# Performance work log

Measured on AMD Instinct MI355X. Metric: run time of the kernel, lower is better.

## Reference

```python
import jax, jax.numpy as jnp
import numpy as np

N, F, DEG, C = 20000, 64, 16, 16   # nodes, features, in-degree incl. self loop, classes
E = N * (DEG - 1)                   # regular (non-self-loop) edges


def setup_inputs() -> dict:
    key = jax.random.key(0)
    ks = jax.random.split(key, 12)
    x = jax.random.normal(ks[0], (N, F), dtype=jnp.float32)
    src = jax.random.randint(ks[1], (E,), 0, N, dtype=jnp.int32)
    dst = jnp.repeat(jnp.arange(N, dtype=jnp.int32), DEG - 1)  # exactly DEG-1 in-edges/node
    edge_index = jnp.stack([src, dst])
    s = 1.0 / np.sqrt(F)
    params = {}
    for i, kw, kb in ((1, ks[2], ks[3]), (2, ks[4], ks[5]), (3, ks[6], ks[7])):
        params[f"W{i}"] = jax.random.normal(kw, (F, F), dtype=jnp.float32) * s
        params[f"b{i}"] = jax.random.normal(kb, (F,), dtype=jnp.float32) * s
    params["Wfc"] = jax.random.normal(ks[8], (C, F), dtype=jnp.float32) * s
    params["bfc"] = jax.random.normal(ks[9], (C,), dtype=jnp.float32) * s
    return {"x": x, "edge_index": edge_index, **params}


def _pca_conv(h, src, dst, W, b):
    # GCNConv.forward: linear first, then propagate with symmetric normalization.
    hl = h @ W.T                                             # [N, F]
    # add self loops (appended after regular edges, as in PyG)
    loop = jnp.arange(N, dtype=src.dtype)
    src_a = jnp.concatenate([src, loop])
    dst_a = jnp.concatenate([dst, loop])
    deg = jnp.zeros((N,), hl.dtype).at[dst_a].add(1.0)
    dinv = jax.lax.rsqrt(deg)
    norm = dinv[src_a] * dinv[dst_a]                         # [Ea]
    m = norm[:, None] * hl[src_a]                            # messages [Ea, F]
    # aggregate(): pack each destination's messages contiguously, in edge order
    order = jnp.argsort(dst_a)                               # stable sort by destination
    sd = dst_a[order]
    slot = jnp.arange(sd.shape[0]) - jnp.searchsorted(sd, sd, side='left')
    neigh = jnp.zeros((N, DEG, F), hl.dtype).at[sd, slot].set(m[order])
    neigh = neigh.reshape(N, DEG * F)                        # [N, max_degree*F]
    # torch.pca_lowrank(neigh, q=F, center=True): top-F right singular vectors of
    # the column-centered matrix; computed via eigh on the (DEG*F x DEG*F) Gram.
    Xc = neigh - jnp.mean(neigh, axis=0, keepdims=True)
    G = Xc.T @ Xc                                            # [DEG*F, DEG*F]
    _, V = jnp.linalg.eigh(G)                                # ascending eigenvalues
    Vtop = V[:, ::-1][:, :F]                                 # top-F principal directions
    proj = neigh @ Vtop                                      # note: projects UNcentered neigh
    return proj @ W.T + b                                    # self.lin again + bias


def reference(x, edge_index, W1, b1, W2, b2, W3, b3, Wfc, bfc):
    src, dst = edge_index[0], edge_index[1]
    h = jax.nn.relu(_pca_conv(x, src, dst, W1, b1))
    h = jax.nn.relu(_pca_conv(h, src, dst, W2, b2))
    h = jax.nn.relu(_pca_conv(h, src, dst, W3, b3))
    out = h @ Wfc.T + bfc
    return jax.nn.log_softmax(out, axis=-1)
```

## Files before the change

kernel.cpp:

```cpp
#include <hip/hip_runtime.h>
#include <cmath>

#define NNODES 20000
#define FD 64
#define EPN 15
#define NB 1024
#define BSUB 80
#define NCLS 16
#define NPAIR 40

__global__ __launch_bounds__(256) void k_linT(const float* __restrict__ X,
    const float* __restrict__ W, const float* __restrict__ bias,
    float* __restrict__ out, int ncol, int relu)
{
  __shared__ float Wsh[64][65];
  __shared__ float Xsh[64][65];
  int t = threadIdx.x;
  int r0 = blockIdx.x * 64;
  for (int idx = t; idx < ncol * 64; idx += 256) Wsh[idx >> 6][idx & 63] = W[idx];
  for (int idx = t; idx < 64 * 64; idx += 256) {
    int r = idx >> 6, c = idx & 63;
    Xsh[r][c] = (r0 + r < NNODES) ? X[(size_t)(r0 + r) * 64 + c] : 0.f;
  }
  __syncthreads();
  for (int idx = t; idx < 64 * ncol; idx += 256) {
    int r = idx / ncol, o = idx % ncol;
    float acc = 0.f;
    #pragma unroll
    for (int j = 0; j < 64; j++) acc += Xsh[r][j] * Wsh[o][j];
    if (bias) acc += bias[o];
    if (relu) acc = fmaxf(acc, 0.f);
    if (r0 + r < NNODES) out[(size_t)(r0 + r) * ncol + o] = acc;
  }
}

__global__ __launch_bounds__(256) void k_meanslot(const float* __restrict__ hl,
    const int* __restrict__ src, float* __restrict__ mus)
{
  int k = blockIdx.x;
  int part = blockIdx.y;
  int t = threadIdx.x;
  int c = t & 63, sub = t >> 6;
  int d0 = part * 2500;
  float acc = 0.f;
  for (int d = d0 + sub; d < d0 + 2500; d += 4) {
    int row = (k < EPN) ? src[d * EPN + k] : d;
    acc += hl[(size_t)row * 64 + c];
  }
  __shared__ float red[4][64];
  red[sub][c] = acc;
  __syncthreads();
  if (t < 64) {
    float s = red[0][t] + red[1][t] + red[2][t] + red[3][t];
    atomicAdd(&mus[k * 64 + t], s * (1.f / 20000.f));
  }
}

__global__ __launch_bounds__(256) void k_buildX(const float* __restrict__ hl,
    const int* __restrict__ src, const float* __restrict__ mus,
    float* __restrict__ X)
{
  __shared__ float4 mu4[256];
  int t = threadIdx.x;
  int d0 = blockIdx.x * 64;
  mu4[t] = ((const float4*)mus)[t];
  __syncthreads();
  for (int k = 0; k < 16; k++) {
    for (int item = t; item < 1024; item += 256) {
      int rr = item >> 4, f4 = item & 15;
      int d = d0 + rr;
      if (d < NNODES) {
        int row = (k < EPN) ? src[d * EPN + k] : d;
        float4 v = ((const float4*)hl)[(size_t)row * 16 + f4];
        float4 m = mu4[k * 16 + f4];
        v.x -= m.x; v.y -= m.y; v.z -= m.z; v.w -= m.w;
        ((float4*)X)[(size_t)d * 256 + k * 16 + f4] = v;
      }
    }
  }
}

__global__ __launch_bounds__(256) void k_syrkX(const float* __restrict__ X,
    float* __restrict__ TP, int rows)
{
  __shared__ float As[32][128];
  __shared__ float Bs[32][128];
  int t = threadIdx.x;
  int pr = blockIdx.x, I = 0, rem = pr;
  for (int ii = 0; ii < 8; ii++) {
    int cnt = 8 - ii;
    if (rem < cnt) { I = ii; break; }
    rem -= cnt;
  }
  int J = I + rem;
  int d0 = blockIdx.y * rows;
  int d1 = d0 + rows;
  int a0 = (t & 15) * 4, b0 = (t >> 4) * 4;
  float4 pa[4], pb[4];
  auto LOADR = [&](int dc) {
    #pragma unroll
    for (int s = 0; s < 4; s++) {
      int idx = t + s * 256;
      int rr = idx >> 5, c4 = idx & 31;
      int d = dc + rr;
      float4 va = make_float4(0.f, 0.f, 0.f, 0.f), vb = va;
      if (d < d1) {
        va = ((const float4*)X)[(size_t)d * 256 + I * 32 + c4];
        vb = ((const float4*)X)[(size_t)d * 256 + J * 32 + c4];
      }
      pa[s] = va; pb[s] = vb;
    }
  };
  LOADR(d0);
  float acc[8][8] = {};
  for (int dc = d0; dc < d1; dc += 32) {
    __syncthreads();
    #pragma unroll
    for (int s = 0; s < 4; s++) {
      int idx = t + s * 256;
      int rr = idx >> 5, c4 = idx & 31;
      *(float4*)&As[rr][c4 * 4] = pa[s];
      *(float4*)&Bs[rr][c4 * 4] = pb[s];
    }
    __syncthreads();
    if (dc + 32 < d1) LOADR(dc + 32);
    for (int dd = 0; dd < 32; dd++) {
      float av[8], bv[8];
      *(float4*)&av[0] = *(const float4*)&As[dd][a0];
      *(float4*)&av[4] = *(const float4*)&As[dd][a0 + 64];
      *(float4*)&bv[0] = *(const float4*)&Bs[dd][b0];
      *(float4*)&bv[4] = *(const float4*)&Bs[dd][b0 + 64];
      #pragma unroll
      for (int x = 0; x < 8; x++)
        #pragma unroll
        for (int y = 0; y < 8; y++) acc[x][y] += av[x] * bv[y];
    }
  }
  float* Tout = TP + (size_t)blockIdx.y * ((size_t)NB * NB);
  #pragma unroll
  for (int x = 0; x < 8; x++) {
    int rowi = I * 128 + ((x < 4) ? (a0 + x) : (64 + a0 + x - 4));
    size_t base = (size_t)rowi * NB + J * 128;
    *(float4*)&Tout[base + b0]      = make_float4(acc[x][0], acc[x][1], acc[x][2], acc[x][3]);
    *(float4*)&Tout[base + 64 + b0] = make_float4(acc[x][4], acc[x][5], acc[x][6], acc[x][7]);
  }
}

__global__ __launch_bounds__(256) void k_assembleG16(const float* __restrict__ TP,
    float* __restrict__ G, int ns, float scale)
{
  size_t idx = (size_t)blockIdx.x * 256 + threadIdx.x;
  int p = (int)(idx >> 10), q = (int)(idx & 1023);
  int ti = p >> 6, tj = q >> 6;
  size_t e = (ti <= tj) ? idx : (((size_t)q << 10) | (size_t)p);
  float v = 0.f;
  for (int s2 = 0; s2 < ns; s2++) v += TP[(size_t)s2 * ((size_t)NB * NB) + e];
  G[idx] = v * scale;
}

__global__ __launch_bounds__(256) void k_gram(const float* __restrict__ hl,
    const int* __restrict__ src, const float* __restrict__ mus,
    float* __restrict__ T)
{
  __shared__ float Ash[64][64];
  __shared__ float Bsh[64][64];
  __shared__ float muA[64], muB[64];
  int t = threadIdx.x;
  int pr = blockIdx.x, i = 0, rem = pr;
  for (int ii = 0; ii < 16; ii++) {
    int cnt = 16 - ii;
    if (rem < cnt) { i = ii; break; }
    rem -= cnt;
  }
  int j = i + rem;
  if (t < 64) muA[t] = mus[i * 64 + t];
  else if (t < 128) muB[t - 64] = mus[j * 64 + (t - 64)];
  float acc[4][4] = {};
  int a0 = (t & 15) * 4, b0 = (t >> 4) * 4;
  int d0 = blockIdx.y * 4000, d1 = d0 + 4000;
  for (int dc = d0; dc < d1; dc += 64) {
    __syncthreads();
    for (int item = t; item < 1024; item += 256) {
      int rr = item >> 4, f4 = item & 15;
      int d = dc + rr;
      float4 va = make_float4(0.f, 0.f, 0.f, 0.f);
      float4 vb = va;
      if (d < d1) {
        int ra = (i < EPN) ? src[d * EPN + i] : d;
        int rb = (j < EPN) ? src[d * EPN + j] : d;
        va = ((const float4*)hl)[(size_t)ra * 16 + f4];
        vb = ((const float4*)hl)[(size_t)rb * 16 + f4];
        int cb = f4 * 4;
        va.x -= muA[cb]; va.y -= muA[cb + 1]; va.z -= muA[cb + 2]; va.w -= muA[cb + 3];
        vb.x -= muB[cb]; vb.y -= muB[cb + 1]; vb.z -= muB[cb + 2]; vb.w -= muB[cb + 3];
      }
      ((float4*)&Ash[rr][0])[f4] = va;
      ((float4*)&Bsh[rr][0])[f4] = vb;
    }
    __syncthreads();
    for (int dd = 0; dd < 64; dd++) {
      float av[4], bv[4];
      #pragma unroll
      for (int u = 0; u < 4; u++) av[u] = Ash[dd][a0 + u];
      #pragma unroll
      for (int u = 0; u < 4; u++) bv[u] = Bsh[dd][b0 + u];
      #pragma unroll
      for (int x = 0; x < 4; x++)
        #pragma unroll
        for (int y = 0; y < 4; y++) acc[x][y] += av[x] * bv[y];
    }
  }
  #pragma unroll
  for (int x = 0; x < 4; x++)
    #pragma unroll
    for (int y = 0; y < 4; y++)
      atomicAdd(&T[(size_t)(i * 64 + a0 + x) * NB + (j * 64 + b0 + y)], acc[x][y]);
}

__global__ __launch_bounds__(256) void k_assembleG(const float* __restrict__ T,
    float* __restrict__ G)
{
  size_t idx = (size_t)blockIdx.x * 256 + threadIdx.x;
  int p = (int)(idx >> 10), q = (int)(idx & 1023);
  int ti = p >> 6, tj = q >> 6;
  float v = (ti <= tj) ? T[idx] : T[((size_t)q << 10) | (size_t)p];
  G[idx] = v * (1.f / 256.f);
}

__global__ __launch_bounds__(256) void k_gemmG2(const float* __restrict__ G,
    float* __restrict__ G2)
{
  __shared__ float Ash[64][68];
  __shared__ float Bsh[64][68];
  int t = threadIdx.x;
  int bi = blockIdx.x * 64, bj = blockIdx.y * 64;
  int a0 = (t & 15) * 4, b0 = (t >> 4) * 4;
  float acc[4][4] = {};
  for (int d0 = 0; d0 < NB; d0 += 64) {
    __syncthreads();
    for (int item = t; item < 1024; item += 256) {
      int rr = item >> 4, f4 = item & 15;
      *(float4*)&Ash[rr][f4 * 4] =
          ((const float4*)G)[(size_t)(d0 + rr) * 256 + (bi >> 2) + f4];
      *(float4*)&Bsh[rr][f4 * 4] =
          ((const float4*)G)[(size_t)(d0 + rr) * 256 + (bj >> 2) + f4];
    }
    __syncthreads();
    for (int dd = 0; dd < 64; dd++) {
      float av[4], bv[4];
      #pragma unroll
      for (int u = 0; u < 4; u++) av[u] = Ash[dd][a0 + u];
      #pragma unroll
      for (int u = 0; u < 4; u++) bv[u] = Bsh[dd][b0 + u];
      #pragma unroll
      for (int x = 0; x < 4; x++)
        #pragma unroll
        for (int y = 0; y < 4; y++) acc[x][y] += av[x] * bv[y];
    }
  }
  #pragma unroll
  for (int x = 0; x < 4; x++) {
    float4 v = make_float4(acc[x][0], acc[x][1], acc[x][2], acc[x][3]);
    ((float4*)G2)[(size_t)(bi + a0 + x) * 256 + ((bj + b0) >> 2)] = v;
  }
}

__global__ void k_initScut(float* __restrict__ S, const float* __restrict__ G,
                           double* __restrict__ scal)
{
  int b = blockIdx.x;
  int t = threadIdx.x;
  if (b == 0) {
    __shared__ float red[256];
    float m = 0.f;
    for (int p = t; p < NB; p += 256) m = fmaxf(m, G[(size_t)p * NB + p]);
    red[t] = m;
    __syncthreads();
    for (int s = 128; s; s >>= 1) {
      if (t < s) red[t] = fmaxf(red[t], red[t + s]);
      __syncthreads();
    }
    if (t == 0) {
      double c = 0.9 * (double)red[0];
      scal[0] = c;
      scal[1] = c * c;
    }
    return;
  }
  int idx = (b - 1) * 256 + t;
  if (idx < NB * BSUB) {
    unsigned u = (unsigned)(idx + 1) * 2654435761u;
    u ^= u >> 16; u *= 2246822519u; u ^= u >> 13; u *= 3266489917u; u ^= u >> 16;
    S[idx] = ((float)u * (1.f / 4294967296.f)) - 0.5f;
  }
}

__global__ __launch_bounds__(256) void k_gzfused(const float* __restrict__ G,
    const float* __restrict__ Z, const float* __restrict__ Zp,
    float* __restrict__ P, float* __restrict__ out, int* __restrict__ cnt,
    const double* __restrict__ cptr, float s1, float s2, float s3)
{
  __shared__ float Gs[32][68];
  __shared__ float Zs[64][84];
  __shared__ int lastf;
  int t = threadIdx.x;
  int r0b = blockIdx.x;
  int r0 = r0b * 32;
  int kz = blockIdx.y;
  int cg_ = t & 15, rg = t >> 4;
  float acc0[5] = {}, acc1[5] = {};
  for (int k0 = kz * 128; k0 < kz * 128 + 128; k0 += 64) {
    __syncthreads();
    #pragma unroll
    for (int s = 0; s < 2; s++) {
      int item = t + s * 256;
      int rr = item >> 4, f4 = item & 15;
      float4 g = ((const float4*)G)[(size_t)(r0 + rr) * 256 + (k0 >> 2) + f4];
      *(float4*)&Gs[rr][f4 * 4] = g;
    }
    #pragma unroll
    for (int s = 0; s < 5; s++) {
      int item = t + s * 256;
      int rr = item / 20, f4 = item % 20;
      float4 z = ((const float4*)Z)[(size_t)(k0 + rr) * 20 + f4];
      *(float4*)&Zs[rr][f4 * 4] = z;
    }
    __syncthreads();
    for (int kk = 0; kk < 64; kk++) {
      float g0 = Gs[rg * 2 + 0][kk];
      float g1 = Gs[rg * 2 + 1][kk];
      float z[5];
      #pragma unroll
      for (int m = 0; m < 5; m++) z[m] = Zs[kk][cg_ * 5 + m];
      #pragma unroll
      for (int m = 0; m < 5; m++) { acc0[m] += g0 * z[m]; acc1[m] += g1 * z[m]; }
    }
  }
  size_t base = (size_t)kz * (NB * BSUB) + (size_t)(r0 + rg * 2) * BSUB + cg_ * 5;
  #pragma unroll
  for (int m = 0; m < 5; m++) P[base + m] = acc0[m];
  #pragma unroll
  for (int m = 0; m < 5; m++) P[base + BSUB + m] = acc1[m];
  __threadfence();
  __syncthreads();
  if (t == 0) {
    int old = atomicAdd(&cnt[r0b], 1);
    lastf = (old == 7) ? 1 : 0;
  }
  __syncthreads();
  if (!lastf) return;
  __threadfence();
  float coef = s1;
  if (cptr) coef = s1 * (float)(2.0 / cptr[0]);
  const float4* P4 = (const float4*)P;
  for (int idx = t; idx < 640; idx += 256) {
    size_t o4 = (size_t)r0 * 20 + idx;
    float4 a = P4[o4];
    #pragma unroll
    for (int u = 1; u < 8; u++) {
      float4 b = P4[(size_t)u * 20480 + o4];
      a.x += b.x; a.y += b.y; a.z += b.z; a.w += b.w;
    }
    float4 z = ((const float4*)Z)[o4];
    float4 o;
    o.x = coef * a.x + s2 * z.x;
    o.y = coef * a.y + s2 * z.y;
    o.z = coef * a.z + s2 * z.z;
    o.w = coef * a.w + s2 * z.w;
    if (s3 != 0.f) {
      float4 zp = ((const float4*)Zp)[o4];
      o.x += s3 * zp.x; o.y += s3 * zp.y; o.z += s3 * zp.z; o.w += s3 * zp.w;
    }
    ((float4*)out)[o4] = o;
  }
  __syncthreads();
  if (t == 0) cnt[r0b] = 0;
}

__global__ __launch_bounds__(512) void k_xtychol(const float* __restrict__ Sa,
    const float* __restrict__ Sb, double* __restrict__ CP,
    float* __restrict__ Rinv, int* __restrict__ cnt)
{
  __shared__ float Xsh[64][BSUB + 1];
  __shared__ float Ysh[64][BSUB + 1];
  __shared__ int lastf;
  int t = threadIdx.x;
  int i0 = blockIdx.x * 64;
  for (int idx = t; idx < 64 * BSUB; idx += 512) {
    int r = idx / BSUB, c = idx % BSUB;
    Xsh[r][c] = Sa[(size_t)(i0 + r) * BSUB + c];
    Ysh[r][c] = Sb[(size_t)(i0 + r) * BSUB + c];
  }
  __syncthreads();
  if (t < 256) {
    int a0 = (t & 15) * 5, b0 = (t >> 4) * 5;
    double acc[5][5] = {};
    for (int dd = 0; dd < 64; dd++) {
      float av[5], bv[5];
      #pragma unroll
      for (int u = 0; u < 5; u++) av[u] = Xsh[dd][a0 + u];
      #pragma unroll
      for (int u = 0; u < 5; u++) bv[u] = Ysh[dd][b0 + u];
      #pragma unroll
      for (int x = 0; x < 5; x++)
        #pragma unroll
        for (int y = 0; y < 5; y++) acc[x][y] += (double)av[x] * (double)bv[y];
    }
    double* outp = CP + (size_t)blockIdx.x * (BSUB * BSUB);
    #pragma unroll
    for (int x = 0; x < 5; x++)
      #pragma unroll
      for (int y = 0; y < 5; y++)
        outp[(size_t)(a0 + x) * BSUB + (b0 + y)] = acc[x][y];
  }
  __threadfence();
  __syncthreads();
  if (t == 0) lastf = (atomicAdd(&cnt[0], 1) == 15) ? 1 : 0;
  __syncthreads();
  if (!lastf) return;
  if (t == 0) cnt[0] = 0;
  __threadfence();
  __shared__ double R[BSUB][BSUB + 1];
  __shared__ double rownew[2][BSUB];
  __shared__ double dinv[BSUB];
  __shared__ float Xi[BSUB][BSUB + 1];
  for (int idx = t; idx < BSUB * BSUB; idx += 512) {
    double s = 0.0;
    #pragma unroll
    for (int b = 0; b < 16; b++) s += CP[(size_t)b * (BSUB * BSUB) + idx];
    R[idx / BSUB][idx % BSUB] = s;
  }
  __syncthreads();
  double flr0 = 1e-30 * (fabs(R[0][0]) + 1e-280);
  int prevrow = -1;
  int pb = 0;
  int k = 0;
  while (k < BSUB - 1) {
    int nrem = BSUB - 1 - k;
    int total = (nrem * (nrem + 1)) >> 1;
    int cplen = (prevrow >= 0) ? (BSUB - prevrow) : 0;
    double piv = R[k][k];
    if (piv < flr0) piv = flr0;
    double rp = 1.0 / piv;
    bool pair = (k + 1 < BSUB - 1);
    if (pair) {
      double dk1 = R[k][k + 1];
      double p1 = R[k + 1][k + 1] - dk1 * dk1 * rp;
      if (p1 < flr0) p1 = flr0;
      double rp1 = 1.0 / p1;
      for (int idx = t; idx < total + cplen; idx += 512) {
        if (idx < total) {
          float nf = 2.f * (float)nrem + 1.f;
          int a = (int)((nf - sqrtf(nf * nf - 8.f * (float)idx)) * 0.5f);
          while (a > 0 && a * nrem - ((a * (a - 1)) >> 1) > idx) a--;
          while ((a + 1) * nrem - (((a + 1) * a) >> 1) <= idx) a++;
          int off = idx - (a * nrem - ((a * (a - 1)) >> 1));
          int i2 = k + 1 + a, j2 = i2 + off;
          if (a == 0) {
            rownew[pb][j2] = R[k + 1][j2] - dk1 * R[k][j2] * rp;
          } else {
            double v = R[i2][j2] - R[k][i2] * R[k][j2] * rp;
            double R1i = R[k + 1][i2] - dk1 * R[k][i2] * rp;
            double R1j = R[k + 1][j2] - dk1 * R[k][j2] * rp;
            v -= R1i * R1j * rp1;
            R[i2][j2] = v;
          }
        } else {
          int j = prevrow + (idx - total);
          R[prevrow][j] = rownew[pb ^ 1][j];
        }
      }
      __syncthreads();
      prevrow = k + 1; pb ^= 1; k += 2;
    } else {
      for (int idx = t; idx < total + cplen; idx += 512) {
        if (idx < total) {
          float nf = 2.f * (float)nrem + 1.f;
          int a = (int)((nf - sqrtf(nf * nf - 8.f * (float)idx)) * 0.5f);
          while (a > 0 && a * nrem - ((a * (a - 1)) >> 1) > idx) a--;
          while ((a + 1) * nrem - (((a + 1) * a) >> 1) <= idx) a++;
          int off = idx - (a * nrem - ((a * (a - 1)) >> 1));
          int i2 = k + 1 + a, j2 = i2 + off;
          R[i2][j2] -= R[k][i2] * R[k][j2] * rp;
        } else {
          int j = prevrow + (idx - total);
          R[prevrow][j] = rownew[pb ^ 1][j];
        }
      }
      __syncthreads();
      prevrow = -1; k += 1;
    }
  }
  if (prevrow >= 0) {
    for (int j = prevrow + t; j < BSUB; j += 512) R[prevrow][j] = rownew[pb ^ 1][j];
    __syncthreads();
  }
  if (t < BSUB) {
    double piv = R[t][t];
    if (piv < flr0) piv = flr0;
    dinv[t] = 1.0 / sqrt(piv);
  }
  __syncthreads();
  for (int idx = t; idx < BSUB * BSUB; idx += 512) {
    int kk = idx / BSUB, j = idx % BSUB;
    if (j > kk) R[kk][j] *= dinv[kk];
  }
  __syncthreads();
  if (t < BSUB) R[t][t] = 1.0 / dinv[t];
  __syncthreads();
  if (t < BSUB) {
    int j = t;
    Xi[j][j] = (float)dinv[j];
    for (int i = j - 1; i >= 0; i--) {
      double s = 0.0;
      for (int k2 = i + 1; k2 <= j; k2++) s += R[i][k2] * (double)Xi[k2][j];
      Xi[i][j] = (float)(-s * dinv[i]);
    }
    for (int i = j + 1; i < BSUB; i++) Xi[i][j] = 0.f;
  }
  __syncthreads();
  for (int idx = t; idx < BSUB * BSUB; idx += 512)
    Rinv[idx] = Xi[idx / BSUB][idx % BSUB];
}

__global__ __launch_bounds__(256) void k_gemmSR(const float* __restrict__ S,
    const float* __restrict__ Rinv, float* __restrict__ out)
{
  __shared__ float Rsh[BSUB][84];
  int t = threadIdx.x;
  for (int idx = t; idx < BSUB * BSUB; idx += 256)
    Rsh[idx / BSUB][idx % BSUB] = Rinv[idx];
  __syncthreads();
  int r0 = blockIdx.x * 32;
  int r = t >> 3, c0 = (t & 7) * 10;
  float acc[10] = {};
  const float* srow = &S[(size_t)(r0 + r) * BSUB];
  for (int k = 0; k < BSUB; k++) {
    float s = srow[k];
    #pragma unroll
    for (int m = 0; m < 10; m++) acc[m] += s * Rsh[k][c0 + m];
  }
  #pragma unroll
  for (int m = 0; m < 10; m++) out[(size_t)(r0 + r) * BSUB + c0 + m] = acc[m];
}

__global__ __launch_bounds__(1024) void k_xtyjac(const float* __restrict__ Sa,
    const float* __restrict__ Sb, double* __restrict__ CP,
    float* __restrict__ Uout, int* __restrict__ perm,
    double* __restrict__ cutout, int sweeps, int withU, int* __restrict__ cnt)
{
  __shared__ float Xsh[64][BSUB + 1];
  __shared__ float Ysh[64][BSUB + 1];
  __shared__ int lastf;
  int t = threadIdx.x;
  int i0 = blockIdx.x * 64;
  for (int idx = t; idx < 64 * BSUB; idx += 1024) {
    int r = idx / BSUB, c = idx % BSUB;
    Xsh[r][c] = Sa[(size_t)(i0 + r) * BSUB + c];
    Ysh[r][c] = Sb[(size_t)(i0 + r) * BSUB + c];
  }
  __syncthreads();
  if (t < 256) {
    int a0 = (t & 15) * 5, b0 = (t >> 4) * 5;
    double acc[5][5] = {};
    for (int dd = 0; dd < 64; dd++) {
      float av[5], bv[5];
      #pragma unroll
      for (int u = 0; u < 5; u++) av[u] = Xsh[dd][a0 + u];
      #pragma unroll
      for (int u = 0; u < 5; u++) bv[u] = Ysh[dd][b0 + u];
      #pragma unroll
      for (int x = 0; x < 5; x++)
        #pragma unroll
        for (int y = 0; y < 5; y++) acc[x][y] += (double)av[x] * (double)bv[y];
    }
    double* outp = CP + (size_t)blockIdx.x * (BSUB * BSUB);
    #pragma unroll
    for (int x = 0; x < 5; x++)
      #pragma unroll
      for (int y = 0; y < 5; y++)
        outp[(size_t)(a0 + x) * BSUB + (b0 + y)] = acc[x][y];
  }
  __threadfence();
  __syncthreads();
  if (t == 0) lastf = (atomicAdd(&cnt[0], 1) == 15) ? 1 : 0;
  __syncthreads();
  if (!lastf) return;
  if (t == 0) cnt[0] = 0;
  __threadfence();
  __shared__ float Mb[2][BSUB][BSUB + 1];
  __shared__ float Ut[BSUB][BSUB];
  __shared__ float4 rot[2][NPAIR];
  __shared__ float th[BSUB];
  __shared__ int id[BSUB];
  for (int idx = t; idx < BSUB * BSUB; idx += 1024) {
    double s = 0.0;
    #pragma unroll
    for (int b = 0; b < 16; b++) s += CP[(size_t)b * (BSUB * BSUB) + idx];
    Mb[1][idx / BSUB][idx % BSUB] = (float)s;
    if (withU) Ut[idx / BSUB][idx % BSUB] = ((idx / BSUB) == (idx % BSUB)) ? 1.f : 0.f;
  }
  int pr0 = t / 40, j0 = t - pr0 * 40;
  int pr1 = -1, j1 = 0;
  {
    int i1 = t + 1024;
    if (i1 < 1600) { pr1 = i1 / 40; j1 = i1 - pr1 * 40; }
  }
  int upr0 = -1, um0 = 0, upr1 = -1, um1 = 0;
  if (t >= 40) {
    int u0 = t - 40;              upr0 = u0 / 40; um0 = u0 - upr0 * 40;
    int u1 = t - 40 + 984;
    if (u1 < 1600) { upr1 = u1 / 40; um1 = u1 - upr1 * 40; }
  }
  int rp_ = 0, rq_ = 0;
  if (t < 40) {
    rp_ = (t == 0) ? 0 : 1 + (t - 1) % 79;
    rq_ = 1 + (78 - t) % 79;
  }
  __syncthreads();
  for (int idx = t; idx < BSUB * BSUB; idx += 1024) {
    int i2 = idx / BSUB, j2 = idx % BSUB;
    Mb[0][i2][j2] = 0.5f * (Mb[1][i2][j2] + Mb[1][j2][i2]);
  }
  __syncthreads();
  int nrounds = sweeps * (BSUB - 1);
  int mcur = 0;
  for (int it = 0; it < nrounds; it++) {
    int pb = it & 1;
    float (*Mc)[BSUB + 1] = Mb[mcur];
    float (*Mn)[BSUB + 1] = Mb[mcur ^ 1];
    if (t < 40) {
      int p = rp_, q = rq_;
      if (p > q) { int tmp = p; p = q; q = tmp; }
      float apq = Mc[p][q];
      float c = 1.f, s = 0.f;
      if (fabsf(apq) > 1e-28f) {
        float tau = (Mc[q][q] - Mc[p][p]) / (2.f * apq);
        float tt = copysignf(1.f, tau) / (fabsf(tau) + sqrtf(1.f + tau * tau));
        c = rsqrtf(1.f + tt * tt);
        s = tt * c;
      }
      rot[pb][t] = make_float4(c, s, __int_as_float(p), __int_as_float(q));
      if (t > 0) rp_ = (rp_ == 79) ? 1 : rp_ + 1;
      rq_ = (rq_ == 79) ? 1 : rq_ + 1;
    } else if (withU && it > 0) {
      int ob = pb ^ 1;
      {
        float4 R0 = rot[ob][upr0];
        int p = __float_as_int(R0.z), q = __float_as_int(R0.w);
        float c = R0.x, s = R0.y;
        float2 up = *(float2*)&Ut[p][2 * um0];
        float2 uq = *(float2*)&Ut[q][2 * um0];
        float2 np, nq;
        np.x = c * up.x - s * uq.x;  np.y = c * up.y - s * uq.y;
        nq.x = s * up.x + c * uq.x;  nq.y = s * up.y + c * uq.y;
        *(float2*)&Ut[p][2 * um0] = np;
        *(float2*)&Ut[q][2 * um0] = nq;
      }
      if (upr1 >= 0) {
        float4 R1 = rot[ob][upr1];
        int p = __float_as_int(R1.z), q = __float_as_int(R1.w);
        float c = R1.x, s = R1.y;
        float2 up = *(float2*)&Ut[p][2 * um1];
        float2 uq = *(float2*)&Ut[q][2 * um1];
        float2 np, nq;
        np.x = c * up.x - s * uq.x;  np.y = c * up.y - s * uq.y;
        nq.x = s * up.x + c * uq.x;  nq.y = s * up.y + c * uq.y;
        *(float2*)&Ut[p][2 * um1] = np;
        *(float2*)&Ut[q][2 * um1] = nq;
      }
    }
    __syncthreads();
    {
      float4 Rp = rot[pb][pr0];
      float4 Rj = rot[pb][j0];
      int p = __float_as_int(Rp.z), q = __float_as_int(Rp.w);
      float c = Rp.x, s = Rp.y;
      int k = __float_as_int(Rj.z), k2 = __float_as_int(Rj.w);
      float cj = Rj.x, sj = Rj.y;
      float mpk = Mc[p][k],  mqk = Mc[q][k];
      float mpk2 = Mc[p][k2], mqk2 = Mc[q][k2];
      float rpk  = c * mpk  - s * mqk;
      float rqk  = s * mpk  + c * mqk;
      float rpk2 = c * mpk2 - s * mqk2;
      float rqk2 = s * mpk2 + c * mqk2;
      Mn[p][k]  = cj * rpk - sj * rpk2;
      Mn[q][k]  = cj * rqk - sj * rqk2;
      Mn[p][k2] = sj * rpk + cj * rpk2;
      Mn[q][k2] = sj * rqk + cj * rqk2;
    }
    if (pr1 >= 0) {
      float4 Rp = rot[pb][pr1];
      float4 Rj = rot[pb][j1];
      int p = __float_as_int(Rp.z), q = __float_as_int(Rp.w);
      float c = Rp.x, s = Rp.y;
      int k = __float_as_int(Rj.z), k2 = __float_as_int(Rj.w);
      float cj = Rj.x, sj = Rj.y;
      float mpk = Mc[p][k],  mqk = Mc[q][k];
      float mpk2 = Mc[p][k2], mqk2 = Mc[q][k2];
      float rpk  = c * mpk  - s * mqk;
      float rqk  = s * mpk  + c * mqk;
      float rpk2 = c * mpk2 - s * mqk2;
      float rqk2 = s * mpk2 + c * mqk2;
      Mn[p][k]  = cj * rpk - sj * rpk2;
      Mn[q][k]  = cj * rqk - sj * rqk2;
      Mn[p][k2] = sj * rpk + cj * rpk2;
      Mn[q][k2] = sj * rqk + cj * rqk2;
    }
    __syncthreads();
    mcur ^= 1;
  }
  if (withU) {
    int ob = (nrounds - 1) & 1;
    {
      float4 R0 = rot[ob][pr0];
      int p = __float_as_int(R0.z), q = __float_as_int(R0.w);
      float c = R0.x, s = R0.y;
      float2 up = *(float2*)&Ut[p][2 * j0];
      float2 uq = *(float2*)&Ut[q][2 * j0];
      float2 np, nq;
      np.x = c * up.x - s * uq.x;  np.y = c * up.y - s * uq.y;
      nq.x = s * up.x + c * uq.x;  nq.y = s * up.y + c * uq.y;
      *(float2*)&Ut[p][2 * j0] = np;
      *(float2*)&Ut[q][2 * j0] = nq;
    }
    if (pr1 >= 0) {
      float4 R1 = rot[ob][pr1];
      int p = __float_as_int(R1.z), q = __float_as_int(R1.w);
      float c = R1.x, s = R1.y;
      float2 up = *(float2*)&Ut[p][2 * j1];
      float2 uq = *(float2*)&Ut[q][2 * j1];
      float2 np, nq;
      np.x = c * up.x - s * uq.x;  np.y = c * up.y - s * uq.y;
      nq.x = s * up.x + c * uq.x;  nq.y = s * up.y + c * uq.y;
      *(float2*)&Ut[p][2 * j1] = np;
      *(float2*)&Ut[q][2 * j1] = nq;
    }
    __syncthreads();
  }
  float (*Mf)[BSUB + 1] = Mb[mcur];
  if (t < BSUB) { th[t] = Mf[t][t]; id[t] = t; }
  __syncthreads();
  if (t == 0) {
    for (int a = 1; a < BSUB; a++) {
      float v = th[a]; int ii = id[a]; int b = a - 1;
      while (b >= 0 && th[b] < v) { th[b + 1] = th[b]; id[b + 1] = id[b]; b--; }
      th[b + 1] = v; id[b + 1] = ii;
    }
    double cut = (double)th[BSUB - 1];
    double lo = 0.02 * (double)th[0];
    if (cut < lo) cut = lo;
    double hi = 0.98 * (double)th[63];
    if (cut > hi) cut = hi;
    cutout[0] = cut;
    cutout[1] = cut * cut;
  }
  __syncthreads();
  if (t < BSUB) perm[t] = id[t];
  if (withU)
    for (int idx = t; idx < BSUB * BSUB; idx += 1024) {
      int k = idx / BSUB, p = idx % BSUB;
      Uout[idx] = Ut[p][k];
    }
}

__global__ __launch_bounds__(256) void k_compose(const float* __restrict__ S,
    const float* __restrict__ U, const int* __restrict__ perm,
    float* __restrict__ out)
{
  __shared__ float Ush[BSUB][65];
  int t = threadIdx.x;
  for (int idx = t; idx < BSUB * 64; idx += 256) {
    int jj = idx >> 6, c = idx & 63;
    Ush[jj][c] = U[jj * BSUB + perm[c]];
  }
  __syncthreads();
  int r0 = blockIdx.x * 64;
  for (int oidx = t; oidx < 64 * 64; oidx += 256) {
    int r = oidx >> 6, c = oidx & 63;
    float acc = 0.f;
    const float* srow = &S[(size_t)(r0 + r) * BSUB];
    #pragma unroll 8
    for (int j = 0; j < BSUB; j++) acc += srow[j] * Ush[j][c];
    out[(size_t)(r0 + r) * 64 + c] = acc;
  }
}

__global__ __launch_bounds__(256) void k_projlin(const float* __restrict__ hl,
    const int* __restrict__ src, const float* __restrict__ Vtop,
    const float* __restrict__ W, const float* __restrict__ bias,
    float* __restrict__ hout)
{
  __shared__ float Vsh[64][68];
  __shared__ float Hsh[64][68];
  __shared__ float Psh[64][68];
  int t = threadIdx.x;
  int d0 = blockIdx.x * 64;
  int dd = t & 63, pg = t >> 6;
  float acc[16] = {};
  for (int k = 0; k < 16; k++) {
    __syncthreads();
    for (int item = t; item < 1024; item += 256) {
      int rr = item >> 4, f4 = item & 15;
      *(float4*)&Vsh[rr][f4 * 4] = ((const float4*)Vtop)[(size_t)(k * 64 + rr) * 16 + f4];
      int d = d0 + rr;
      float4 v = make_float4(0.f, 0.f, 0.f, 0.f);
      if (d < NNODES) {
        int row = (k < EPN) ? src[d * EPN + k] : d;
        v = ((const float4*)hl)[(size_t)row * 16 + f4];
      }
      *(float4*)&Hsh[rr][f4 * 4] = v;
    }
    __syncthreads();
    for (int j = 0; j < 64; j++) {
      float h = Hsh[dd][j];
      #pragma unroll
      for (int m = 0; m < 16; m++) acc[m] += h * Vsh[j][pg * 16 + m];
    }
  }
  __syncthreads();
  #pragma unroll
  for (int m = 0; m < 16; m++) Psh[dd][pg * 16 + m] = acc[m] * (1.f / 16.f);
  for (int item = t; item < 1024; item += 256) {
    int rr = item >> 4, f4 = item & 15;
    *(float4*)&Vsh[rr][f4 * 4] = ((const float4*)W)[(size_t)rr * 16 + f4];
  }
  __syncthreads();
  if (d0 + dd < NNODES) {
    #pragma unroll
    for (int m = 0; m < 16; m++) {
      int o = pg * 16 + m;
      float a = bias[o];
      for (int j = 0; j < 64; j++) a += Psh[dd][j] * Vsh[o][j];
      hout[(size_t)(d0 + dd) * 64 + o] = fmaxf(a, 0.f);
    }
  }
}

__global__ void k_logsoftmax(const float* __restrict__ logits, float* __restrict__ out)
{
  int n = blockIdx.x * 256 + threadIdx.x;
  if (n >= NNODES) return;
  float v[NCLS];
  float mx = -1e30f;
  #pragma unroll
  for (int c = 0; c < NCLS; c++) { v[c] = logits[(size_t)n * NCLS + c]; mx = fmaxf(mx, v[c]); }
  float se = 0.f;
  #pragma unroll
  for (int c = 0; c < NCLS; c++) se += expf(v[c] - mx);
  float lse = mx + logf(se);
  #pragma unroll
  for (int c = 0; c < NCLS; c++) out[(size_t)n * NCLS + c] = v[c] - lse;
}

extern "C" void kernel_launch(void* const* d_in, const int* in_sizes, int n_in,
                              void* d_out, int out_size, void* d_ws, size_t ws_size,
                              hipStream_t stream)
{
  (void)in_sizes; (void)n_in; (void)out_size;
  const float* x = (const float*)d_in[0];
  const int* src = (const int*)d_in[1];
  const float* Wl[3] = { (const float*)d_in[2], (const float*)d_in[4], (const float*)d_in[6] };
  const float* bl[3] = { (const float*)d_in[3], (const float*)d_in[5], (const float*)d_in[7] };
  const float* Wfc = (const float*)d_in[8];
  const float* bfc = (const float*)d_in[9];
  float* outp = (float*)d_out;

  char* w = (char*)d_ws;
  auto alloc = [&](size_t bytes) -> char* {
    char* p = w; w += (bytes + 255) & ~(size_t)255; return p;
  };
  float* hA   = (float*)alloc((size_t)NNODES * 64 * 4);
  float* hB   = (float*)alloc((size_t)NNODES * 64 * 4);
  float* hl   = (float*)alloc((size_t)NNODES * 64 * 4);
  float* T    = (float*)alloc((size_t)NB * NB * 4);
  float* G    = (float*)alloc((size_t)NB * NB * 4);
  float* G2   = (float*)alloc((size_t)NB * NB * 4);
  float* mus  = (float*)alloc(16 * 64 * 4);
  float* Zb[6];
  for (int i = 0; i < 6; i++) Zb[i] = (float*)alloc((size_t)NB * BSUB * 4);
  float* P     = (float*)alloc((size_t)8 * NB * BSUB * 4);
  int* cnt     = (int*)alloc(64 * 4);
  double* CP   = (double*)alloc((size_t)16 * BSUB * BSUB * 8);
  float* Rinv  = (float*)alloc(BSUB * BSUB * 4);
  float* U     = (float*)alloc(BSUB * BSUB * 4);
  int* perm    = (int*)alloc(BSUB * 4);
  float* Vtop  = (float*)alloc((size_t)NB * 64 * 4);
  double* scal = (double*)alloc(16 * 8);
  float* X      = (float*)alloc((size_t)NNODES * NB * 4);
  float* TP     = (float*)alloc((size_t)16 * (size_t)NB * NB * 4);
  size_t used16 = (size_t)(w - (char*)d_ws);
  (void)alloc((size_t)4 * (size_t)NB * NB * 4);
  size_t used20 = (size_t)(w - (char*)d_ws);
  int fastg = (used16 <= ws_size) ? 1 : 0;
  int NS    = (used20 <= ws_size) ? 20 : 16;

  const int GRID_ROWS = (NNODES + 63) / 64;

  hipMemsetAsync(cnt, 0, 64 * 4, stream);

  int cur = 0;
  auto gemmGZ = [&](const float* A, const float* Z, const float* Zp, float* o,
                    const double* cptr, float s1, float s2, float s3) {
    hipLaunchKernelGGL(k_gzfused, dim3(32, 8), dim3(256), 0, stream,
                       A, Z, Zp, P, o, cnt, cptr, s1, s2, s3);
  };
  auto chunk2 = [&](int deg, const double* cptr) {
    int a = (cur + 1) % 6, b = (cur + 2) % 6;
    float* bufs[3] = { Zb[cur], Zb[a], Zb[b] };
    int ip = 0, ic = 0, io = 1;
    for (int s = 0; s < deg; s++) {
      if (s == 0)
        gemmGZ(G2, bufs[ic], nullptr, bufs[io], cptr, 1.f, -1.f, 0.f);
      else
        gemmGZ(G2, bufs[ic], bufs[ip], bufs[io], cptr, 2.f, -2.f, -1.f);
      if (s == 0) { ip = 0; ic = 1; io = 2; }
      else { int tmp = ip; ip = ic; ic = io; io = tmp; }
    }
    int sel = (deg - 1) % 3;
    cur = (sel == 0) ? a : (sel == 1) ? b : cur;
  };
  auto cholqr = [&]() {
    hipLaunchKernelGGL(k_xtychol, dim3(16), dim3(512), 0, stream,
                       Zb[cur], Zb[cur], CP, Rinv, cnt + 32);
    int o = (cur + 1) % 6;
    hipLaunchKernelGGL(k_gemmSR, dim3(32), dim3(256), 0, stream, Zb[cur], Rinv, Zb[o]);
    cur = o;
  };
  auto rrmid = [&](double* cutp) {
    int y = (cur + 1) % 6;
    gemmGZ(G, Zb[cur], nullptr, Zb[y], nullptr, 1.f, 0.f, 0.f);
    hipLaunchKernelGGL(k_xtyjac, dim3(16), dim3(1024), 0, stream,
                       Zb[cur], Zb[y], CP, U, perm, cutp, 2, 0, cnt + 33);
  };
  auto rrfinal = [&](double* cutp) {
    int y = (cur + 1) % 6;
    gemmGZ(G, Zb[cur], nullptr, Zb[y], nullptr, 1.f, 0.f, 0.f);
    hipLaunchKernelGGL(k_xtyjac, dim3(16), dim3(1024), 0, stream,
                       Zb[cur], Zb[y], CP, U, perm, cutp, 5, 1, cnt + 33);
    hipLaunchKernelGGL(k_compose, dim3(16), dim3(256), 0, stream,
                       Zb[cur], U, perm, Vtop);
  };

  const float* hin = x;
  float* hout = hA;
  for (int l = 0; l < 3; l++) {
    hipLaunchKernelGGL(k_linT, dim3(GRID_ROWS), dim3(256), 0, stream,
                       hin, Wl[l], (const float*)nullptr, hl, 64, 0);
    hipMemsetAsync(mus, 0, 16 * 64 * 4, stream);
    hipLaunchKernelGGL(k_meanslot, dim3(16, 8), dim3(256), 0, stream, hl, src, mus);
    if (fastg) {
      hipLaunchKernelGGL(k_buildX, dim3(GRID_ROWS), dim3(256), 0, stream,
                         hl, src, mus, X);
      hipLaunchKernelGGL(k_syrkX, dim3(36, NS), dim3(256), 0, stream,
                         X, TP, NNODES / NS);
      hipLaunchKernelGGL(k_assembleG16, dim3(4096), dim3(256), 0, stream,
                         TP, G, NS, 1.f / 256.f);
      hipLaunchKernelGGL(k_syrkX, dim3(36, 4), dim3(256), 0, stream,
                         G, TP, NB / 4);
      hipLaunchKernelGGL(k_assembleG16, dim3(4096), dim3(256), 0, stream,
                         TP, G2, 4, 1.f);
    } else {
      hipMemsetAsync(T, 0, (size_t)NB * NB * 4, stream);
      hipLaunchKernelGGL(k_gram, dim3(136, 5), dim3(256), 0, stream, hl, src, mus, T);
      hipLaunchKernelGGL(k_assembleG, dim3(4096), dim3(256), 0, stream, T, G);
      hipLaunchKernelGGL(k_gemmG2, dim3(16, 16), dim3(256), 0, stream, G, G2);
    }
    cur = 0;
    hipLaunchKernelGGL(k_initScut, dim3(1 + (NB * BSUB + 255) / 256), dim3(256), 0,
                       stream, Zb[cur], G, scal);
    chunk2(6, &scal[1]); cholqr();
    rrmid(&scal[2]);
    chunk2(7, &scal[3]); cholqr();
    chunk2(7, &scal[3]); cholqr();
    rrfinal(&scal[4]);
    hipLaunchKernelGGL(k_projlin, dim3(GRID_ROWS), dim3(256), 0, stream,
                       hl, src, Vtop, Wl[l], bl[l], hout);
    hin = hout;
    hout = (hout == hA) ? hB : hA;
  }
  hipLaunchKernelGGL(k_linT, dim3(GRID_ROWS), dim3(256), 0, stream,
                     hin, Wfc, bfc, hl, NCLS, 0);
  hipLaunchKernelGGL(k_logsoftmax, dim3((NNODES + 255) / 256), dim3(256), 0, stream,
                     hl, outp);
}
```

Measured before the change: 8.858 ms.

## Store uncentered neighbor matrix, subtract means in syrk, fuse init into assemble

The neighbor matrix X is now built uncentered. Slot means are computed from X by a new contiguous-read kernel, and the mean is subtracted inside the syrk tile loads. Because X is uncentered, k_projlin can read X directly instead of re-gathering rows of hl through src indices. The random-init and diagonal-max setup kernel is folded into extra blocks of the second assemble launch, saving a launch. The cost is an extra per-element subtraction in syrk and a 2D-strided mean read over the large X buffer.

New measurement: 8.683 ms. 1.02x faster.

```diff
diff --git a/kernel.cpp b/kernel.cpp
--- a/kernel.cpp
+++ b/kernel.cpp
@@ -56,15 +56,31 @@
   }
 }
 
+__global__ __launch_bounds__(256) void k_meanslotX(const float* __restrict__ X,
+    float* __restrict__ mus)
+{
+  int k = blockIdx.x;
+  int part = blockIdx.y;
+  int t = threadIdx.x;
+  int c = t & 63, sub = t >> 6;
+  int d0 = part * 2500;
+  float acc = 0.f;
+  for (int d = d0 + sub; d < d0 + 2500; d += 4)
+    acc += X[(size_t)d * 1024 + k * 64 + c];
+  __shared__ float red[4][64];
+  red[sub][c] = acc;
+  __syncthreads();
+  if (t < 64) {
+    float s = red[0][t] + red[1][t] + red[2][t] + red[3][t];
+    atomicAdd(&mus[k * 64 + t], s * (1.f / 20000.f));
+  }
+}
+
 __global__ __launch_bounds__(256) void k_buildX(const float* __restrict__ hl,
-    const int* __restrict__ src, const float* __restrict__ mus,
-    float* __restrict__ X)
-{
-  __shared__ float4 mu4[256];
+    const int* __restrict__ src, float* __restrict__ X)
+{
   int t = threadIdx.x;
   int d0 = blockIdx.x * 64;
-  mu4[t] = ((const float4*)mus)[t];
-  __syncthreads();
   for (int k = 0; k < 16; k++) {
     for (int item = t; item < 1024; item += 256) {
       int rr = item >> 4, f4 = item & 15;
@@ -72,8 +88,6 @@
       if (d < NNODES) {
         int row = (k < EPN) ? src[d * EPN + k] : d;
         float4 v = ((const float4*)hl)[(size_t)row * 16 + f4];
-        float4 m = mu4[k * 16 + f4];
-        v.x -= m.x; v.y -= m.y; v.z -= m.z; v.w -= m.w;
         ((float4*)X)[(size_t)d * 256 + k * 16 + f4] = v;
       }
     }
@@ -81,10 +95,11 @@
 }
 
 __global__ __launch_bounds__(256) void k_syrkX(const float* __restrict__ X,
-    float* __restrict__ TP, int rows)
+    float* __restrict__ TP, int rows, const float* __restrict__ mus)
 {
   __shared__ float As[32][128];
   __shared__ float Bs[32][128];
+  __shared__ float muA[128], muB[128];
   int t = threadIdx.x;
   int pr = blockIdx.x, I = 0, rem = pr;
   for (int ii = 0; ii < 8; ii++) {
@@ -93,6 +108,9 @@
     rem -= cnt;
   }
   int J = I + rem;
+  if (t < 128) muA[t] = mus ? mus[I * 128 + t] : 0.f;
+  else muB[t - 128] = mus ? mus[J * 128 + (t - 128)] : 0.f;
+  __syncthreads();
   int d0 = blockIdx.y * rows;
   int d1 = d0 + rows;
   int a0 = (t & 15) * 4, b0 = (t >> 4) * 4;
@@ -107,6 +125,10 @@
       if (d < d1) {
         va = ((const float4*)X)[(size_t)d * 256 + I * 32 + c4];
         vb = ((const float4*)X)[(size_t)d * 256 + J * 32 + c4];
+        float4 ma = *(const float4*)&muA[c4 * 4];
+        float4 mb = *(const float4*)&muB[c4 * 4];
+        va.x -= ma.x; va.y -= ma.y; va.z -= ma.z; va.w -= ma.w;
+        vb.x -= mb.x; vb.y -= mb.y; vb.z -= mb.z; vb.w -= mb.w;
       }
       pa[s] = va; pb[s] = vb;
     }
@@ -147,9 +169,39 @@
 }
 
 __global__ __launch_bounds__(256) void k_assembleG16(const float* __restrict__ TP,
-    float* __restrict__ G, int ns, float scale)
-{
-  size_t idx = (size_t)blockIdx.x * 256 + threadIdx.x;
+    float* __restrict__ G, int ns, float scale,
+    float* __restrict__ Sinit, const float* __restrict__ Gd,
+    double* __restrict__ scal)
+{
+  int b = blockIdx.x;
+  int t = threadIdx.x;
+  if (b >= 4096) {
+    if (b == 4096) {
+      __shared__ float red[256];
+      float m = 0.f;
+      for (int p = t; p < NB; p += 256) m = fmaxf(m, Gd[(size_t)p * NB + p]);
+      red[t] = m;
+      __syncthreads();
+      for (int s = 128; s; s >>= 1) {
+        if (t < s) red[t] = fmaxf(red[t], red[t + s]);
+        __syncthreads();
+      }
+      if (t == 0) {
+        double c = 0.9 * (double)red[0];
+        scal[0] = c;
+        scal[1] = c * c;
+      }
+    } else {
+      int idx = (b - 4097) * 256 + t;
+      if (idx < NB * BSUB) {
+        unsigned u = (unsigned)(idx + 1) * 2654435761u;
+        u ^= u >> 16; u *= 2246822519u; u ^= u >> 13; u *= 3266489917u; u ^= u >> 16;
+        Sinit[idx] = ((float)u * (1.f / 4294967296.f)) - 0.5f;
+      }
+    }
+    return;
+  }
+  size_t idx = (size_t)b * 256 + t;
   int p = (int)(idx >> 10), q = (int)(idx & 1023);
   int ti = p >> 6, tj = q >> 6;
   size_t e = (ti <= tj) ? idx : (((size_t)q << 10) | (size_t)p);
@@ -789,7 +841,7 @@
 __global__ __launch_bounds__(256) void k_projlin(const float* __restrict__ hl,
     const int* __restrict__ src, const float* __restrict__ Vtop,
     const float* __restrict__ W, const float* __restrict__ bias,
-    float* __restrict__ hout)
+    float* __restrict__ hout, const float* __restrict__ Xmat)
 {
   __shared__ float Vsh[64][68];
   __shared__ float Hsh[64][68];
@@ -806,8 +858,12 @@
       int d = d0 + rr;
       float4 v = make_float4(0.f, 0.f, 0.f, 0.f);
       if (d < NNODES) {
-        int row = (k < EPN) ? src[d * EPN + k] : d;
-        v = ((const float4*)hl)[(size_t)row * 16 + f4];
+        if (Xmat) {
+          v = ((const float4*)Xmat)[(size_t)d * 256 + k * 16 + f4];
+        } else {
+          int row = (k < EPN) ? src[d * EPN + k] : d;
+          v = ((const float4*)hl)[(size_t)row * 16 + f4];
+        }
       }
       *(float4*)&Hsh[rr][f4 * 4] = v;
     }
@@ -948,34 +1004,38 @@
     hipLaunchKernelGGL(k_linT, dim3(GRID_ROWS), dim3(256), 0, stream,
                        hin, Wl[l], (const float*)nullptr, hl, 64, 0);
     hipMemsetAsync(mus, 0, 16 * 64 * 4, stream);
-    hipLaunchKernelGGL(k_meanslot, dim3(16, 8), dim3(256), 0, stream, hl, src, mus);
     if (fastg) {
       hipLaunchKernelGGL(k_buildX, dim3(GRID_ROWS), dim3(256), 0, stream,
-                         hl, src, mus, X);
+                         hl, src, X);
+      hipLaunchKernelGGL(k_meanslotX, dim3(16, 8), dim3(256), 0, stream, X, mus);
       hipLaunchKernelGGL(k_syrkX, dim3(36, NS), dim3(256), 0, stream,
-                         X, TP, NNODES / NS);
+                         X, TP, NNODES / NS, mus);
       hipLaunchKernelGGL(k_assembleG16, dim3(4096), dim3(256), 0, stream,
-                         TP, G, NS, 1.f / 256.f);
+                         TP, G, NS, 1.f / 256.f,
+                         (float*)nullptr, (const float*)nullptr, (double*)nullptr);
       hipLaunchKernelGGL(k_syrkX, dim3(36, 4), dim3(256), 0, stream,
-                         G, TP, NB / 4);
-      hipLaunchKernelGGL(k_assembleG16, dim3(4096), dim3(256), 0, stream,
-                         TP, G2, 4, 1.f);
+                         G, TP, NB / 4, (const float*)nullptr);
+      cur = 0;
+      hipLaunchKernelGGL(k_assembleG16, dim3(4096 + 1 + 320), dim3(256), 0, stream,
+                         TP, G2, 4, 1.f, Zb[cur], G, scal);
     } else {
+      hipLaunchKernelGGL(k_meanslot, dim3(16, 8), dim3(256), 0, stream, hl, src, mus);
       hipMemsetAsync(T, 0, (size_t)NB * NB * 4, stream);
       hipLaunchKernelGGL(k_gram, dim3(136, 5), dim3(256), 0, stream, hl, src, mus, T);
       hipLaunchKernelGGL(k_assembleG, dim3(4096), dim3(256), 0, stream, T, G);
       hipLaunchKernelGGL(k_gemmG2, dim3(16, 16), dim3(256), 0, stream, G, G2);
-    }
-    cur = 0;
-    hipLaunchKernelGGL(k_initScut, dim3(1 + (NB * BSUB + 255) / 256), dim3(256), 0,
-                       stream, Zb[cur], G, scal);
+      cur = 0;
+      hipLaunchKernelGGL(k_initScut, dim3(1 + (NB * BSUB + 255) / 256), dim3(256), 0,
+                         stream, Zb[cur], G, scal);
+    }
     chunk2(6, &scal[1]); cholqr();
     rrmid(&scal[2]);
     chunk2(7, &scal[3]); cholqr();
     chunk2(7, &scal[3]); cholqr();
     rrfinal(&scal[4]);
     hipLaunchKernelGGL(k_projlin, dim3(GRID_ROWS), dim3(256), 0, stream,
-                       hl, src, Vtop, Wl[l], bl[l], hout);
+                       hl, src, Vtop, Wl[l], bl[l], hout,
+                       fastg ? (const float*)X : (const float*)nullptr);
     hin = hout;
     hout = (hout == hA) ? hB : hA;
   }
```
